# Optimization experiments

Measured on AMD Instinct MI355X. Metric: run time of the kernel, lower is better.

Reference implementation:

```python
import jax, jax.numpy as jnp
import numpy as np

NUM_HEADS = 16

def setup_inputs() -> dict:
    key = jax.random.key(0)
    ks = jax.random.split(key, 4)
    D = 1024
    x = jax.random.normal(ks[0], (2, 8192, D), dtype=jnp.float32)
    s = 1.0 / np.sqrt(D)
    Wqkv = jax.random.normal(ks[1], (D, 3 * D), dtype=jnp.float32) * s
    Wq = jax.random.normal(ks[2], (D, D), dtype=jnp.float32) * s
    Wproj = jax.random.normal(ks[3], (D, D), dtype=jnp.float32) * s
    return {
        "x": x,
        "Wqkv": Wqkv, "bqkv": jnp.zeros((3 * D,), jnp.float32),
        "Wq": Wq, "bq": jnp.zeros((D,), jnp.float32),
        "Wproj": Wproj, "bproj": jnp.zeros((D,), jnp.float32),
        "num_anchor_tokens": 1024,
    }

def reference(x, Wqkv, bqkv, Wq, bq, Wproj, bproj, num_anchor_tokens):
    B, S, D = x.shape
    H = NUM_HEADS
    hd = D // H
    A = num_anchor_tokens
    scale = 1.0 / jnp.sqrt(jnp.float32(hd))

    anchors = x[:, :A, :]          # (B, A, D)
    queries = x[:, A:, :]          # (B, Sq, D)
    Sq = S - A

    # Anchor QKV projection: (B, A, 3, H, hd)
    aqkv = (anchors @ Wqkv + bqkv).reshape(B, A, 3, H, hd)
    aqkv = jnp.transpose(aqkv, (2, 0, 3, 1, 4))   # (3, B, H, A, hd)
    aq, ak, av = aqkv[0], aqkv[1], aqkv[2]

    # Query-token Q projection: (B, H, Sq, hd)
    qq = (queries @ Wq + bq).reshape(B, Sq, H, hd)
    qq = jnp.transpose(qq, (0, 2, 1, 3))

    q = jnp.concatenate([aq, qq], axis=2)         # (B, H, S, hd)

    # All queries attend only to anchor keys/values
    scores = jnp.einsum('bhqd,bhkd->bhqk', q, ak) * scale   # (B, H, S, A)
    attn = jax.nn.softmax(scores, axis=-1)
    out = jnp.einsum('bhqk,bhkd->bhqd', attn, av)           # (B, H, S, hd)

    out = jnp.transpose(out, (0, 2, 1, 3)).reshape(B, S, D)
    return out @ Wproj + bproj
```

## Files before the change

kernel.cpp:

```cpp
#include <hip/hip_runtime.h>
#include <cstdint>

#define B_ 2
#define S_ 8192
#define D_ 1024
#define H_ 16
#define HD_ 64
#define A_ 1024
#define SQ_ 7168

#define QSCALE 0.18033688011112042f

typedef unsigned short ushort_t;
typedef unsigned int uint_t;
typedef __bf16 bf16x8 __attribute__((ext_vector_type(8)));
typedef float floatx4 __attribute__((ext_vector_type(4)));
typedef ushort_t ushort8 __attribute__((ext_vector_type(8)));
typedef uint_t uint2v __attribute__((ext_vector_type(2)));

__device__ __forceinline__ ushort_t f2bf(float f) {
  uint_t u = __builtin_bit_cast(uint_t, f);
  u += 0x7fffu + ((u >> 16) & 1u);
  return (ushort_t)(u >> 16);
}
__device__ __forceinline__ float bf2f(ushort_t h) {
  uint_t u = ((uint_t)h) << 16;
  return __builtin_bit_cast(float, u);
}

__device__ __forceinline__ void glds16(const ushort_t* g, ushort_t* l) {
  __builtin_amdgcn_global_load_lds(
      (const __attribute__((address_space(1))) void*)g,
      (__attribute__((address_space(3))) void*)l, 16, 0, 0);
}

__global__ __launch_bounds__(256) void cvt_x(const float* __restrict__ x,
                                             ushort_t* __restrict__ xb) {
  int i = (blockIdx.x * 256 + threadIdx.x) * 8;
  float4 a = *(const float4*)(x + i);
  float4 b = *(const float4*)(x + i + 4);
  ushort8 o;
  o[0] = f2bf(a.x); o[1] = f2bf(a.y); o[2] = f2bf(a.z); o[3] = f2bf(a.w);
  o[4] = f2bf(b.x); o[5] = f2bf(b.y); o[6] = f2bf(b.z); o[7] = f2bf(b.w);
  *(ushort8*)(xb + i) = o;
}

__global__ __launch_bounds__(256) void cvt_wT(const float* __restrict__ W,
                                              ushort_t* __restrict__ WT, int N) {
  __shared__ float t[32][33];
  int n0 = blockIdx.x * 32, k0 = blockIdx.y * 32;
  int tx = threadIdx.x, ty = threadIdx.y;
  #pragma unroll
  for (int i = ty; i < 32; i += 8) t[i][tx] = W[(uint64_t)(k0 + i) * N + n0 + tx];
  __syncthreads();
  #pragma unroll
  for (int i = ty; i < 32; i += 8)
    WT[(uint64_t)(n0 + i) * 1024 + k0 + tx] = f2bf(t[tx][i]);
}

template <int MODE>
__global__ __launch_bounds__(256) void gemm_bt(
    const ushort_t* __restrict__ Abase, const ushort_t* __restrict__ WT,
    const float* __restrict__ bias,
    ushort_t* __restrict__ Qb, ushort_t* __restrict__ Kb,
    ushort_t* __restrict__ Vb, float* __restrict__ outf) {
  __shared__ __align__(16) ushort_t At[128 * 32];
  __shared__ __align__(16) ushort_t Bt[128 * 32];
  const int t = threadIdx.x;
  const int lane = t & 63;
  const int quad = lane >> 4, ln = lane & 15;
  const int wave = t >> 6;
  const int wm = wave & 1, wn = wave >> 1;
  const int m0 = blockIdx.x * 128, n0 = blockIdx.y * 128;

  const int r0 = t >> 2, seg = t & 3;
  auto maprow = [&](int gm) -> int {
    if (MODE == 0) { int b = gm >> 10; int a = gm & 1023; return b * S_ + a; }
    if (MODE == 1) { int b = (gm >= SQ_) ? 1 : 0; int sq = gm - b * SQ_; return b * S_ + A_ + sq; }
    return gm;
  };
  const ushort_t* arow0 = Abase + (uint64_t)maprow(m0 + r0) * 1024;
  const ushort_t* arow1 = Abase + (uint64_t)maprow(m0 + 64 + r0) * 1024;
  const ushort_t* brow0 = WT + (uint64_t)(n0 + r0) * 1024;
  const ushort_t* brow1 = WT + (uint64_t)(n0 + 64 + r0) * 1024;
  ushort_t* At_lo = (ushort_t*)((char*)At + wave * 1024);
  ushort_t* At_hi = (ushort_t*)((char*)At + 4096 + wave * 1024);
  ushort_t* Bt_lo = (ushort_t*)((char*)Bt + wave * 1024);
  ushort_t* Bt_hi = (ushort_t*)((char*)Bt + 4096 + wave * 1024);

  floatx4 acc[4][4];
  #pragma unroll
  for (int i = 0; i < 4; ++i)
    #pragma unroll
    for (int j = 0; j < 4; ++j) acc[i][j] = (floatx4)0.0f;

  for (int k0 = 0; k0 < 1024; k0 += 32) {
    __syncthreads();
    glds16(arow0 + k0 + seg * 8, At_lo);
    glds16(arow1 + k0 + seg * 8, At_hi);
    glds16(brow0 + k0 + seg * 8, Bt_lo);
    glds16(brow1 + k0 + seg * 8, Bt_hi);
    __syncthreads();
    bf16x8 af[4], bfr[4];
    #pragma unroll
    for (int i = 0; i < 4; ++i)
      af[i] = *(const bf16x8*)&At[(wm * 64 + i * 16 + ln) * 32 + quad * 8];
    #pragma unroll
    for (int j = 0; j < 4; ++j)
      bfr[j] = *(const bf16x8*)&Bt[(wn * 64 + j * 16 + ln) * 32 + quad * 8];
    #pragma unroll
    for (int i = 0; i < 4; ++i)
      #pragma unroll
      for (int j = 0; j < 4; ++j)
        acc[i][j] = __builtin_amdgcn_mfma_f32_16x16x32_bf16(af[i], bfr[j], acc[i][j], 0, 0, 0);
  }

  #pragma unroll
  for (int i = 0; i < 4; ++i) {
    #pragma unroll
    for (int j = 0; j < 4; ++j) {
      #pragma unroll
      for (int r = 0; r < 4; ++r) {
        int gm = m0 + wm * 64 + i * 16 + quad * 4 + r;
        int gn = n0 + wn * 64 + j * 16 + ln;
        float v = acc[i][j][r] + bias[gn];
        if (MODE == 2) {
          outf[(uint64_t)gm * 1024 + gn] = v;
        } else if (MODE == 0) {
          int b = gm >> 10, a = gm & 1023;
          int which = gn >> 10, h = (gn >> 6) & 15, d = gn & 63;
          if (which == 0)
            Qb[((uint64_t)(b * H_ + h) * S_ + a) * HD_ + d] = f2bf(v * QSCALE);
          else if (which == 1)
            Kb[((uint64_t)(b * H_ + h) * A_ + a) * HD_ + d] = f2bf(v);
          else
            Vb[((uint64_t)(b * H_ + h) * HD_ + d) * A_ + a] = f2bf(v);
        } else {
          int b = (gm >= SQ_) ? 1 : 0; int sq = gm - b * SQ_;
          int h = gn >> 6, d = gn & 63;
          Qb[((uint64_t)(b * H_ + h) * S_ + (A_ + sq)) * HD_ + d] = f2bf(v * QSCALE);
        }
      }
    }
  }
}

__global__ __launch_bounds__(256) void attn_mfma(const ushort_t* __restrict__ Qb,
                                                 const ushort_t* __restrict__ Kb,
                                                 const ushort_t* __restrict__ Vb,
                                                 ushort_t* __restrict__ Ob) {
  __shared__ __align__(16) ushort_t Ks[64 * 72];
  __shared__ __align__(16) ushort_t Vt[80 * 72];
  __shared__ __align__(16) ushort_t Ps[128 * 72];
  const int t = threadIdx.x;
  const int lane = t & 63;
  const int quad = lane >> 4, ln = lane & 15;
  const int wave = t >> 6;
  const int wm = wave & 1, wn = wave >> 1;
  const int bh = blockIdx.y;
  const int b = bh >> 4, h = bh & 15;
  const int m0 = blockIdx.x * 128;

  bf16x8 qf[4][2];
  {
    const ushort_t* qbase = Qb + ((uint64_t)bh * S_ + m0 + wn * 64 + ln) * HD_ + quad * 8;
    #pragma unroll
    for (int j = 0; j < 4; ++j)
      #pragma unroll
      for (int ks = 0; ks < 2; ++ks)
        qf[j][ks] = *(const bf16x8*)(qbase + (uint64_t)(j * 16) * HD_ + ks * 32);
  }
  if (t < 64) Vt[64 * 72 + t] = 0x3F80;

  floatx4 oacc[2][5];
  #pragma unroll
  for (int i = 0; i < 2; ++i)
    #pragma unroll
    for (int j = 0; j < 5; ++j) oacc[i][j] = (floatx4)0.0f;

  const ushort_t* kcbase = Kb + (uint64_t)bh * A_ * HD_;
  const ushort_t* vcbase = Vb + (uint64_t)bh * HD_ * A_;
  const int srow = t >> 2, sseg = t & 3;

  for (int kc = 0; kc < 16; ++kc) {
    const ushort_t* kg = kcbase + (uint64_t)(kc * 64 + srow) * 64 + sseg * 16;
    const ushort_t* vg = vcbase + (uint64_t)srow * A_ + kc * 64 + sseg * 16;
    ushort8 k0 = *(const ushort8*)kg;
    ushort8 k1 = *(const ushort8*)(kg + 8);
    ushort8 v0 = *(const ushort8*)vg;
    ushort8 v1 = *(const ushort8*)(vg + 8);
    __syncthreads();
    *(ushort8*)&Ks[srow * 72 + sseg * 16] = k0;
    *(ushort8*)&Ks[srow * 72 + sseg * 16 + 8] = k1;
    *(ushort8*)&Vt[srow * 72 + sseg * 16] = v0;
    *(ushort8*)&Vt[srow * 72 + sseg * 16 + 8] = v1;
    __syncthreads();

    floatx4 sacc[2][4];
    #pragma unroll
    for (int i = 0; i < 2; ++i)
      #pragma unroll
      for (int j = 0; j < 4; ++j) sacc[i][j] = (floatx4)0.0f;
    #pragma unroll
    for (int ks = 0; ks < 2; ++ks) {
      bf16x8 kf[2];
      #pragma unroll
      for (int i = 0; i < 2; ++i)
        kf[i] = *(const bf16x8*)&Ks[(wm * 32 + i * 16 + ln) * 72 + ks * 32 + quad * 8];
      #pragma unroll
      for (int i = 0; i < 2; ++i)
        #pragma unroll
        for (int j = 0; j < 4; ++j)
          sacc[i][j] = __builtin_amdgcn_mfma_f32_16x16x32_bf16(kf[i], qf[j][ks], sacc[i][j], 0, 0, 0);
    }
    #pragma unroll
    for (int i = 0; i < 2; ++i)
      #pragma unroll
      for (int j = 0; j < 4; ++j) {
        float p0 = __builtin_amdgcn_exp2f(sacc[i][j][0]);
        float p1 = __builtin_amdgcn_exp2f(sacc[i][j][1]);
        float p2 = __builtin_amdgcn_exp2f(sacc[i][j][2]);
        float p3 = __builtin_amdgcn_exp2f(sacc[i][j][3]);
        uint_t lo = (uint_t)f2bf(p0) | ((uint_t)f2bf(p1) << 16);
        uint_t hi = (uint_t)f2bf(p2) | ((uint_t)f2bf(p3) << 16);
        uint2v pk; pk[0] = lo; pk[1] = hi;
        int q = wn * 64 + j * 16 + ln;
        int key = wm * 32 + i * 16 + quad * 4;
        *(uint2v*)&Ps[q * 72 + key] = pk;
      }
    __syncthreads();

    #pragma unroll
    for (int ks = 0; ks < 2; ++ks) {
      bf16x8 af[2];
      #pragma unroll
      for (int i2 = 0; i2 < 2; ++i2)
        af[i2] = *(const bf16x8*)&Ps[(wave * 32 + i2 * 16 + ln) * 72 + ks * 32 + quad * 8];
      bf16x8 bv[5];
      #pragma unroll
      for (int j = 0; j < 5; ++j)
        bv[j] = *(const bf16x8*)&Vt[(j * 16 + ln) * 72 + ks * 32 + quad * 8];
      #pragma unroll
      for (int i2 = 0; i2 < 2; ++i2)
        #pragma unroll
        for (int j = 0; j < 5; ++j)
          oacc[i2][j] = __builtin_amdgcn_mfma_f32_16x16x32_bf16(af[i2], bv[j], oacc[i2][j], 0, 0, 0);
    }
  }

  #pragma unroll
  for (int i2 = 0; i2 < 2; ++i2) {
    #pragma unroll
    for (int r = 0; r < 4; ++r) {
      float lsum = __shfl(oacc[i2][4][r], lane & 48);
      float inv = 1.0f / lsum;
      int qrow = m0 + wave * 32 + i2 * 16 + quad * 4 + r;
      ushort_t* op = Ob + ((uint64_t)b * S_ + qrow) * D_ + h * HD_;
      #pragma unroll
      for (int j = 0; j < 4; ++j)
        op[j * 16 + ln] = f2bf(oacc[i2][j][r] * inv);
    }
  }
}

extern "C" void kernel_launch(void* const* d_in, const int* in_sizes, int n_in,
                              void* d_out, int out_size, void* d_ws, size_t ws_size,
                              hipStream_t stream) {
  (void)in_sizes; (void)n_in; (void)out_size; (void)ws_size;
  const float* x     = (const float*)d_in[0];
  const float* Wqkv  = (const float*)d_in[1];
  const float* bqkv  = (const float*)d_in[2];
  const float* Wq    = (const float*)d_in[3];
  const float* bq    = (const float*)d_in[4];
  const float* Wproj = (const float*)d_in[5];
  const float* bproj = (const float*)d_in[6];
  float* out = (float*)d_out;

  char* ws = (char*)d_ws;
  ushort_t* xb     = (ushort_t*)ws; ws += (size_t)B_ * S_ * D_ * 2;
  ushort_t* wqkvT  = (ushort_t*)ws; ws += (size_t)3 * D_ * D_ * 2;
  ushort_t* wqT    = (ushort_t*)ws; ws += (size_t)D_ * D_ * 2;
  ushort_t* wprojT = (ushort_t*)ws; ws += (size_t)D_ * D_ * 2;
  ushort_t* Qb     = (ushort_t*)ws; ws += (size_t)B_ * H_ * S_ * HD_ * 2;
  ushort_t* Kb     = (ushort_t*)ws; ws += (size_t)B_ * H_ * A_ * HD_ * 2;
  ushort_t* Vb     = (ushort_t*)ws; ws += (size_t)B_ * H_ * A_ * HD_ * 2;
  ushort_t* Ob     = (ushort_t*)ws;

  cvt_x<<<dim3((B_ * S_ * D_) / (256 * 8)), dim3(256), 0, stream>>>(x, xb);
  cvt_wT<<<dim3(3072 / 32, 32), dim3(32, 8), 0, stream>>>(Wqkv, wqkvT, 3072);
  cvt_wT<<<dim3(1024 / 32, 32), dim3(32, 8), 0, stream>>>(Wq, wqT, 1024);
  cvt_wT<<<dim3(1024 / 32, 32), dim3(32, 8), 0, stream>>>(Wproj, wprojT, 1024);

  gemm_bt<0><<<dim3((B_ * A_) / 128, 3072 / 128), dim3(256), 0, stream>>>(
      xb, wqkvT, bqkv, Qb, Kb, Vb, nullptr);
  gemm_bt<1><<<dim3((B_ * SQ_) / 128, 1024 / 128), dim3(256), 0, stream>>>(
      xb, wqT, bq, Qb, nullptr, nullptr, nullptr);
  attn_mfma<<<dim3(S_ / 128, B_ * H_), dim3(256), 0, stream>>>(Qb, Kb, Vb, Ob);
  gemm_bt<2><<<dim3((B_ * S_) / 128, 1024 / 128), dim3(256), 0, stream>>>(
      Ob, wprojT, bproj, nullptr, nullptr, nullptr, out);
}
```

Measured before the change: 378.3 us.

## Merge weight conversions into one launch, use native bf16 casts, add setprio

```diff
diff --git a/kernel.cpp b/kernel.cpp
--- a/kernel.cpp
+++ b/kernel.cpp
@@ -14,6 +14,7 @@
 typedef unsigned short ushort_t;
 typedef unsigned int uint_t;
 typedef __bf16 bf16x8 __attribute__((ext_vector_type(8)));
+typedef __bf16 bf16x4 __attribute__((ext_vector_type(4)));
 typedef float floatx4 __attribute__((ext_vector_type(4)));
 typedef ushort_t ushort8 __attribute__((ext_vector_type(8)));
 typedef uint_t uint2v __attribute__((ext_vector_type(2)));
@@ -23,9 +24,9 @@
   u += 0x7fffu + ((u >> 16) & 1u);
   return (ushort_t)(u >> 16);
 }
-__device__ __forceinline__ float bf2f(ushort_t h) {
-  uint_t u = ((uint_t)h) << 16;
-  return __builtin_bit_cast(float, u);
+__device__ __forceinline__ ushort_t f2bf_c(float f) {
+  __bf16 h = (__bf16)f;
+  return __builtin_bit_cast(ushort_t, h);
 }
 
 __device__ __forceinline__ void glds16(const ushort_t* g, ushort_t* l) {
@@ -40,22 +41,32 @@
   float4 a = *(const float4*)(x + i);
   float4 b = *(const float4*)(x + i + 4);
   ushort8 o;
-  o[0] = f2bf(a.x); o[1] = f2bf(a.y); o[2] = f2bf(a.z); o[3] = f2bf(a.w);
-  o[4] = f2bf(b.x); o[5] = f2bf(b.y); o[6] = f2bf(b.z); o[7] = f2bf(b.w);
+  o[0] = f2bf_c(a.x); o[1] = f2bf_c(a.y); o[2] = f2bf_c(a.z); o[3] = f2bf_c(a.w);
+  o[4] = f2bf_c(b.x); o[5] = f2bf_c(b.y); o[6] = f2bf_c(b.z); o[7] = f2bf_c(b.w);
   *(ushort8*)(xb + i) = o;
 }
 
-__global__ __launch_bounds__(256) void cvt_wT(const float* __restrict__ W,
-                                              ushort_t* __restrict__ WT, int N) {
+__global__ __launch_bounds__(256) void cvt_w_all(
+    const float* __restrict__ Wqkv, const float* __restrict__ Wq,
+    const float* __restrict__ Wproj, ushort_t* __restrict__ wqkvT,
+    ushort_t* __restrict__ wqT, ushort_t* __restrict__ wprojT) {
   __shared__ float t[32][33];
+  const int z = blockIdx.z;
+  const float* W;
+  ushort_t* WT;
+  int stride, colofs;
+  if (z < 3)      { W = Wqkv;  WT = wqkvT + (size_t)z * 1024 * 1024; stride = 3072; colofs = z * 1024; }
+  else if (z == 3){ W = Wq;    WT = wqT;    stride = 1024; colofs = 0; }
+  else            { W = Wproj; WT = wprojT; stride = 1024; colofs = 0; }
   int n0 = blockIdx.x * 32, k0 = blockIdx.y * 32;
   int tx = threadIdx.x, ty = threadIdx.y;
   #pragma unroll
-  for (int i = ty; i < 32; i += 8) t[i][tx] = W[(uint64_t)(k0 + i) * N + n0 + tx];
+  for (int i = ty; i < 32; i += 8)
+    t[i][tx] = W[(uint64_t)(k0 + i) * stride + colofs + n0 + tx];
   __syncthreads();
   #pragma unroll
   for (int i = ty; i < 32; i += 8)
-    WT[(uint64_t)(n0 + i) * 1024 + k0 + tx] = f2bf(t[tx][i]);
+    WT[(uint64_t)(n0 + i) * 1024 + k0 + tx] = f2bf_c(t[tx][i]);
 }
 
 template <int MODE>
@@ -130,15 +141,15 @@
           int b = gm >> 10, a = gm & 1023;
           int which = gn >> 10, h = (gn >> 6) & 15, d = gn & 63;
           if (which == 0)
-            Qb[((uint64_t)(b * H_ + h) * S_ + a) * HD_ + d] = f2bf(v * QSCALE);
+            Qb[((uint64_t)(b * H_ + h) * S_ + a) * HD_ + d] = f2bf_c(v * QSCALE);
           else if (which == 1)
-            Kb[((uint64_t)(b * H_ + h) * A_ + a) * HD_ + d] = f2bf(v);
+            Kb[((uint64_t)(b * H_ + h) * A_ + a) * HD_ + d] = f2bf_c(v);
           else
-            Vb[((uint64_t)(b * H_ + h) * HD_ + d) * A_ + a] = f2bf(v);
+            Vb[((uint64_t)(b * H_ + h) * HD_ + d) * A_ + a] = f2bf_c(v);
         } else {
           int b = (gm >= SQ_) ? 1 : 0; int sq = gm - b * SQ_;
           int h = gn >> 6, d = gn & 63;
-          Qb[((uint64_t)(b * H_ + h) * S_ + (A_ + sq)) * HD_ + d] = f2bf(v * QSCALE);
+          Qb[((uint64_t)(b * H_ + h) * S_ + (A_ + sq)) * HD_ + d] = f2bf_c(v * QSCALE);
         }
       }
     }
@@ -201,6 +212,7 @@
     for (int i = 0; i < 2; ++i)
       #pragma unroll
       for (int j = 0; j < 4; ++j) sacc[i][j] = (floatx4)0.0f;
+    __builtin_amdgcn_s_setprio(1);
     #pragma unroll
     for (int ks = 0; ks < 2; ++ks) {
       bf16x8 kf[2];
@@ -213,6 +225,7 @@
         for (int j = 0; j < 4; ++j)
           sacc[i][j] = __builtin_amdgcn_mfma_f32_16x16x32_bf16(kf[i], qf[j][ks], sacc[i][j], 0, 0, 0);
     }
+    __builtin_amdgcn_s_setprio(0);
     #pragma unroll
     for (int i = 0; i < 2; ++i)
       #pragma unroll
@@ -221,15 +234,16 @@
         float p1 = __builtin_amdgcn_exp2f(sacc[i][j][1]);
         float p2 = __builtin_amdgcn_exp2f(sacc[i][j][2]);
         float p3 = __builtin_amdgcn_exp2f(sacc[i][j][3]);
-        uint_t lo = (uint_t)f2bf(p0) | ((uint_t)f2bf(p1) << 16);
-        uint_t hi = (uint_t)f2bf(p2) | ((uint_t)f2bf(p3) << 16);
-        uint2v pk; pk[0] = lo; pk[1] = hi;
+        bf16x4 pv;
+        pv[0] = (__bf16)p0; pv[1] = (__bf16)p1;
+        pv[2] = (__bf16)p2; pv[3] = (__bf16)p3;
         int q = wn * 64 + j * 16 + ln;
         int key = wm * 32 + i * 16 + quad * 4;
-        *(uint2v*)&Ps[q * 72 + key] = pk;
+        *(bf16x4*)&Ps[q * 72 + key] = pv;
       }
     __syncthreads();
 
+    __builtin_amdgcn_s_setprio(1);
     #pragma unroll
     for (int ks = 0; ks < 2; ++ks) {
       bf16x8 af[2];
@@ -246,6 +260,7 @@
         for (int j = 0; j < 5; ++j)
           oacc[i2][j] = __builtin_amdgcn_mfma_f32_16x16x32_bf16(af[i2], bv[j], oacc[i2][j], 0, 0, 0);
     }
+    __builtin_amdgcn_s_setprio(0);
   }
 
   #pragma unroll
@@ -258,7 +273,7 @@
       ushort_t* op = Ob + ((uint64_t)b * S_ + qrow) * D_ + h * HD_;
       #pragma unroll
       for (int j = 0; j < 4; ++j)
-        op[j * 16 + ln] = f2bf(oacc[i2][j][r] * inv);
+        op[j * 16 + ln] = f2bf_c(oacc[i2][j][r] * inv);
     }
   }
 }
@@ -287,9 +302,8 @@
   ushort_t* Ob     = (ushort_t*)ws;
 
   cvt_x<<<dim3((B_ * S_ * D_) / (256 * 8)), dim3(256), 0, stream>>>(x, xb);
-  cvt_wT<<<dim3(3072 / 32, 32), dim3(32, 8), 0, stream>>>(Wqkv, wqkvT, 3072);
-  cvt_wT<<<dim3(1024 / 32, 32), dim3(32, 8), 0, stream>>>(Wq, wqT, 1024);
-  cvt_wT<<<dim3(1024 / 32, 32), dim3(32, 8), 0, stream>>>(Wproj, wprojT, 1024);
+  cvt_w_all<<<dim3(32, 32, 5), dim3(32, 8), 0, stream>>>(
+      Wqkv, Wq, Wproj, wqkvT, wqT, wprojT);
 
   gemm_bt<0><<<dim3((B_ * A_) / 128, 3072 / 128), dim3(256), 0, stream>>>(
       xb, wqkvT, bqkv, Qb, Kb, Vb, nullptr);
```

Result: no change. 373.4 us (-1.3%).
